# Kernel tuning notes

Hardware: AMD Instinct MI355X
Metric: run time of the kernel (lower is better)

## Reference

```python
import jax, jax.numpy as jnp
import numpy as np

BATCH, NUM_SPEC, VOCAB = 64, 8, 128000


def setup_inputs() -> dict:
    key = jax.random.key(0)
    k1, k2, k3 = jax.random.split(key, 3)
    target_logits = jax.random.normal(k1, (BATCH, NUM_SPEC, VOCAB), dtype=jnp.float32)
    draft_token_ids = jax.random.randint(k2, (BATCH, NUM_SPEC), 0, VOCAB, dtype=jnp.int64)
    bonus_token_ids = jax.random.randint(k3, (BATCH, 1), 0, VOCAB, dtype=jnp.int64)
    return {
        'target_logits': target_logits,
        'draft_token_ids': draft_token_ids,
        'bonus_token_ids': bonus_token_ids,
    }


def reference(target_logits, draft_token_ids, bonus_token_ids):
    # Greedy rejection sampling (speculative decoding).
    batch_size, num_spec = draft_token_ids.shape
    # argmax over vocab -> target tokens  [B, S]
    target_token_ids = jnp.argmax(target_logits, axis=-1).astype(draft_token_ids.dtype)

    masks = draft_token_ids == target_token_ids                      # [B, S]
    rng = jnp.arange(num_spec)[None, :]                              # [1, S]
    # equals[i, j] True iff all drafts up to j matched (prefix of accepts)
    equals = (jnp.cumsum(masks.astype(jnp.int32), axis=1) - 1) == rng  # [B, S]
    num_rejected_tokens = num_spec - jnp.sum(equals, axis=1)
    first_diff_indices = jnp.argmin(equals.astype(jnp.int32), axis=1, keepdims=True)  # [B, 1]
    keeps = (rng <= first_diff_indices) | equals                     # [B, S]
    keep_token_ids = jnp.where(keeps, target_token_ids, -1)          # [B, S]
    keep_bonus_ids = jnp.where(equals[:, -1:], bonus_token_ids, -1)  # [B, 1]
    output_token_ids = jnp.concatenate([keep_token_ids, keep_bonus_ids], axis=1)  # [B, S+1]
    keep_all = jnp.concatenate([keeps, equals[:, -1:]], axis=1)      # [B, S+1]
    last_indices = jnp.cumsum(keep_all.astype(jnp.int32), axis=1)[:, -1] - 1  # [B]
    last_token_ids = output_token_ids[jnp.arange(batch_size), last_indices]
    return output_token_ids, num_rejected_tokens, last_token_ids
```

## Files before the change

kernel.cpp:

```cpp
#include <hip/hip_runtime.h>

constexpr int BATCH    = 64;
constexpr int NUM_SPEC = 8;
constexpr int VOCAB    = 128000;
constexpr int ROWS     = BATCH * NUM_SPEC;
constexpr int T1       = 1024;

typedef float vfloat4 __attribute__((ext_vector_type(4)));

__device__ __forceinline__ void nt_load(vfloat4& dst, int voff, const float* sbase) {
    asm volatile("global_load_dwordx4 %0, %1, %2 nt"
                 : "=v"(dst) : "v"(voff), "s"(sbase));
}
__device__ __forceinline__ void wait_vm4(vfloat4& a, vfloat4& b, vfloat4& c, vfloat4& d) {
    asm volatile("s_waitcnt vmcnt(4)" : "+v"(a), "+v"(b), "+v"(c), "+v"(d));
}
__device__ __forceinline__ void wait_vm0(vfloat4& a, vfloat4& b, vfloat4& c, vfloat4& d) {
    asm volatile("s_waitcnt vmcnt(0)" : "+v"(a), "+v"(b), "+v"(c), "+v"(d));
}

__global__ __launch_bounds__(T1, 8) void rs_argmax(const float* __restrict__ logits,
                                                   int* __restrict__ targets) {
    const int row = blockIdx.x;
    const int tid = threadIdx.x;
    const float* __restrict__ basef = logits + (size_t)row * VOCAB;

    const int voff0 = tid << 4;
    const int voff1 = voff0 + 16384;
    const int voff2 = voff0 + 32768;
    const int voff3 = voff0 + 49152;
    const bool has4  = (tid < 256);
    const int voff3t = has4 ? voff3 : voff0;

    float best = -__builtin_inff();
    int   bidx = VOCAB;

    auto upd = [&](const vfloat4 v, const int vecidx) {
        const int base = vecidx << 2;
        if (v.x > best) { best = v.x; bidx = base;     }
        if (v.y > best) { best = v.y; bidx = base + 1; }
        if (v.z > best) { best = v.z; bidx = base + 2; }
        if (v.w > best) { best = v.w; bidx = base + 3; }
    };
    auto consume = [&](const int j, const vfloat4 v0, const vfloat4 v1,
                       const vfloat4 v2, const vfloat4 v3) {
        const int jb = tid + j * 4096;
        upd(v0, jb);
        upd(v1, jb + 1024);
        upd(v2, jb + 2048);
        upd(v3, jb + 3072);
    };

    vfloat4 A0, A1, A2, A3, B0, B1, B2, B3;

    nt_load(A0, voff0, basef);
    nt_load(A1, voff1, basef);
    nt_load(A2, voff2, basef);
    nt_load(A3, voff3, basef);
    nt_load(B0, voff0, basef + 1 * 16384);
    nt_load(B1, voff1, basef + 1 * 16384);
    nt_load(B2, voff2, basef + 1 * 16384);
    nt_load(B3, voff3, basef + 1 * 16384);

    wait_vm4(A0, A1, A2, A3);  consume(0, A0, A1, A2, A3);
    nt_load(A0, voff0, basef + 2 * 16384);
    nt_load(A1, voff1, basef + 2 * 16384);
    nt_load(A2, voff2, basef + 2 * 16384);
    nt_load(A3, voff3, basef + 2 * 16384);

    wait_vm4(B0, B1, B2, B3);  consume(1, B0, B1, B2, B3);
    nt_load(B0, voff0, basef + 3 * 16384);
    nt_load(B1, voff1, basef + 3 * 16384);
    nt_load(B2, voff2, basef + 3 * 16384);
    nt_load(B3, voff3, basef + 3 * 16384);

    wait_vm4(A0, A1, A2, A3);  consume(2, A0, A1, A2, A3);
    nt_load(A0, voff0, basef + 4 * 16384);
    nt_load(A1, voff1, basef + 4 * 16384);
    nt_load(A2, voff2, basef + 4 * 16384);
    nt_load(A3, voff3, basef + 4 * 16384);

    wait_vm4(B0, B1, B2, B3);  consume(3, B0, B1, B2, B3);
    nt_load(B0, voff0, basef + 5 * 16384);
    nt_load(B1, voff1, basef + 5 * 16384);
    nt_load(B2, voff2, basef + 5 * 16384);
    nt_load(B3, voff3, basef + 5 * 16384);

    wait_vm4(A0, A1, A2, A3);  consume(4, A0, A1, A2, A3);
    nt_load(A0, voff0, basef + 6 * 16384);
    nt_load(A1, voff1, basef + 6 * 16384);
    nt_load(A2, voff2, basef + 6 * 16384);
    nt_load(A3, voff3, basef + 6 * 16384);

    wait_vm4(B0, B1, B2, B3);  consume(5, B0, B1, B2, B3);
    nt_load(B0, voff0,  basef + 7 * 16384);
    nt_load(B1, voff1,  basef + 7 * 16384);
    nt_load(B2, voff2,  basef + 7 * 16384);
    nt_load(B3, voff3t, basef + 7 * 16384);

    wait_vm4(A0, A1, A2, A3);  consume(6, A0, A1, A2, A3);

    wait_vm0(B0, B1, B2, B3);
    {
        const int jb = tid + 7 * 4096;
        upd(B0, jb);
        upd(B1, jb + 1024);
        upd(B2, jb + 2048);
        if (has4) upd(B3, jb + 3072);
    }

    #pragma unroll
    for (int off = 32; off > 0; off >>= 1) {
        const float ov = __shfl_down(best, off, 64);
        const int   oi = __shfl_down(bidx, off, 64);
        if (ov > best || (ov == best && oi < bidx)) { best = ov; bidx = oi; }
    }

    __shared__ float sval[T1 / 64];
    __shared__ int   sidx[T1 / 64];
    const int lane = tid & 63;
    const int wave = tid >> 6;
    if (lane == 0) { sval[wave] = best; sidx[wave] = bidx; }
    __syncthreads();

    if (tid == 0) {
        best = sval[0]; bidx = sidx[0];
        #pragma unroll
        for (int w = 1; w < T1 / 64; ++w) {
            if (sval[w] > best || (sval[w] == best && sidx[w] < bidx)) {
                best = sval[w]; bidx = sidx[w];
            }
        }
        targets[row] = bidx;
    }
}

__global__ __launch_bounds__(64) void rs_finalize(const int* __restrict__ targets,
                                                  const int* __restrict__ draft,
                                                  const int* __restrict__ bonus,
                                                  int* __restrict__ out) {
    const int b = threadIdx.x;
    if (b >= BATCH) return;

    int tgt[NUM_SPEC];
    int L = 0;
    bool prefix = true;
    #pragma unroll
    for (int s = 0; s < NUM_SPEC; ++s) {
        tgt[s] = targets[b * NUM_SPEC + s];
        const bool m = (draft[b * NUM_SPEC + s] == tgt[s]);
        prefix = prefix && m;
        if (prefix) ++L;
    }

    const bool all_acc = (L == NUM_SPEC);
    const int keep_cnt = all_acc ? NUM_SPEC : (L + 1);

    int* __restrict__ out_tok = out + b * (NUM_SPEC + 1);
    #pragma unroll
    for (int s = 0; s < NUM_SPEC; ++s) {
        out_tok[s] = (s < keep_cnt) ? tgt[s] : -1;
    }
    const int bonus_tok = bonus[b];
    out_tok[NUM_SPEC] = all_acc ? bonus_tok : -1;

    out[BATCH * (NUM_SPEC + 1) + b] = NUM_SPEC - L;
    out[BATCH * (NUM_SPEC + 1) + BATCH + b] = all_acc ? bonus_tok
                                                      : tgt[L];
}

extern "C" void kernel_launch(void* const* d_in, const int* in_sizes, int n_in,
                              void* d_out, int out_size, void* d_ws, size_t ws_size,
                              hipStream_t stream) {
    const float* logits = (const float*)d_in[0];
    const int*   draft  = (const int*)d_in[1];
    const int*   bonus  = (const int*)d_in[2];
    int* out = (int*)d_out;
    int* targets = (int*)d_ws;

    rs_argmax<<<ROWS, T1, 0, stream>>>(logits, targets);
    rs_finalize<<<1, 64, 0, stream>>>(targets, draft, bonus, out);
}
```

Baseline: 330.4 us.

## Fuse finalize into argmax kernel via per-batch last-block atomic counter

Removes the separate finalize launch. After writing its argmax, each row's block bumps a per-batch atomic counter, and the eighth block to arrive does the rejection and output logic using atomically read targets. The goal is to cut the second launch and its dependency gap. The counter is only reset through a CAS against a 0xAAAAAAAA poison value and is never cleared after use, so repeated calls are only correct if the workspace is re-poisoned or zeroed each time.

Measured after the change: 353.6 us. 1.07x slower.

```diff
diff --git a/kernel.cpp b/kernel.cpp
--- a/kernel.cpp
+++ b/kernel.cpp
@@ -19,8 +19,12 @@
     asm volatile("s_waitcnt vmcnt(0)" : "+v"(a), "+v"(b), "+v"(c), "+v"(d));
 }
 
-__global__ __launch_bounds__(T1, 8) void rs_argmax(const float* __restrict__ logits,
-                                                   int* __restrict__ targets) {
+__global__ __launch_bounds__(T1, 8) void rs_fused(const float* __restrict__ logits,
+                                                  const int* __restrict__ draft,
+                                                  const int* __restrict__ bonus,
+                                                  int* __restrict__ out,
+                                                  int* __restrict__ targets,
+                                                  unsigned* __restrict__ cnt) {
     const int row = blockIdx.x;
     const int tid = threadIdx.x;
     const float* __restrict__ basef = logits + (size_t)row * VOCAB;
@@ -123,36 +127,39 @@
     if (lane == 0) { sval[wave] = best; sidx[wave] = bidx; }
     __syncthreads();
 
-    if (tid == 0) {
-        best = sval[0]; bidx = sidx[0];
-        #pragma unroll
-        for (int w = 1; w < T1 / 64; ++w) {
-            if (sval[w] > best || (sval[w] == best && sidx[w] < bidx)) {
-                best = sval[w]; bidx = sidx[w];
-            }
+    if (tid != 0) return;
+
+    best = sval[0]; bidx = sidx[0];
+    #pragma unroll
+    for (int w = 1; w < T1 / 64; ++w) {
+        if (sval[w] > best || (sval[w] == best && sidx[w] < bidx)) {
+            best = sval[w]; bidx = sidx[w];
         }
-        targets[row] = bidx;
     }
-}
+    targets[row] = bidx;
 
-__global__ __launch_bounds__(64) void rs_finalize(const int* __restrict__ targets,
-                                                  const int* __restrict__ draft,
-                                                  const int* __restrict__ bonus,
-                                                  int* __restrict__ out) {
-    const int b = threadIdx.x;
-    if (b >= BATCH) return;
+    __threadfence();
+    const int b = row >> 3;
+    unsigned* cb = cnt + b;
+    atomicCAS(cb, 0xAAAAAAAAu, 0u);
+    const unsigned old = atomicAdd(cb, 1u);
+    if (old != NUM_SPEC - 1) return;
 
+    __threadfence();
     int tgt[NUM_SPEC];
-    int L = 0;
-    bool prefix = true;
     #pragma unroll
     for (int s = 0; s < NUM_SPEC; ++s) {
-        tgt[s] = targets[b * NUM_SPEC + s];
+        const int r = (b << 3) | s;
+        tgt[s] = (r == row) ? bidx : atomicAdd(&targets[r], 0);
+    }
+
+    int L = 0; bool prefix = true;
+    #pragma unroll
+    for (int s = 0; s < NUM_SPEC; ++s) {
         const bool m = (draft[b * NUM_SPEC + s] == tgt[s]);
         prefix = prefix && m;
         if (prefix) ++L;
     }
-
     const bool all_acc = (L == NUM_SPEC);
     const int keep_cnt = all_acc ? NUM_SPEC : (L + 1);
 
@@ -176,8 +183,8 @@
     const int*   draft  = (const int*)d_in[1];
     const int*   bonus  = (const int*)d_in[2];
     int* out = (int*)d_out;
-    int* targets = (int*)d_ws;
+    int*      targets = (int*)d_ws;
+    unsigned* cnt     = (unsigned*)d_ws + 512;
 
-    rs_argmax<<<ROWS, T1, 0, stream>>>(logits, targets);
-    rs_finalize<<<1, 64, 0, stream>>>(targets, draft, bonus, out);
+    rs_fused<<<ROWS, T1, 0, stream>>>(logits, draft, bonus, out, targets, cnt);
 }
```
